# Performance work log

Measured on AMD Instinct MI355X. Metric: run time of the kernel, lower is better.

Reference implementation:

```python
import jax, jax.numpy as jnp
import numpy as np

SEQ, B, D_IN, D_H = 1024, 64, 256, 256


def setup_inputs() -> dict:
    key = jax.random.key(0)
    ks = jax.random.split(key, 9)
    scale = 1.0 / np.sqrt(D_IN + D_H)
    inputs = jax.random.normal(ks[0], (SEQ, B, D_IN), dtype=jnp.float32)
    def lin(k):
        kw, kb = jax.random.split(k)
        W = jax.random.uniform(kw, (D_IN + D_H, D_H), jnp.float32, -scale, scale)
        b = jax.random.uniform(kb, (D_H,), jnp.float32, -scale, scale)
        return W, b
    Wf, bf = lin(ks[1])
    Wi, bi = lin(ks[2])
    Wg, bg = lin(ks[3])
    Wo, bo = lin(ks[4])
    return {"inputs": inputs, "Wf": Wf, "bf": bf, "Wi": Wi, "bi": bi,
            "Wg": Wg, "bg": bg, "Wo": Wo, "bo": bo}


def reference(inputs, Wf, bf, Wi, bi, Wg, bg, Wo, bo):
    B_ = inputs.shape[1]
    hx0 = jnp.zeros((B_, D_H), dtype=inputs.dtype)
    cx0 = jnp.zeros((B_, D_H), dtype=inputs.dtype)

    def step(carry, x):
        hx, cx = carry
        comb = jnp.concatenate([x, hx], axis=1)  # [B, D_IN + D_H]
        f = jax.nn.sigmoid(comb @ Wf + bf)
        i = jax.nn.sigmoid(comb @ Wi + bi)
        g = jnp.tanh(comb @ Wg + bg)
        o = jax.nn.sigmoid(comb @ Wo + bo)
        cx = f * cx + i * g
        hx = o * jnp.tanh(cx)
        return (hx, cx), hx

    (hx, cx), outputs = jax.lax.scan(step, (hx0, cx0), inputs)
    return outputs, hx, cx
```

## Files before the change

kernel.cpp:

```cpp
#include <hip/hip_runtime.h>
#include <hip/hip_bf16.h>


typedef _Float16 f16;
typedef _Float16 f16x4 __attribute__((ext_vector_type(4)));
typedef _Float16 f16x8 __attribute__((ext_vector_type(8)));
typedef float f32x4 __attribute__((ext_vector_type(4)));
typedef int i32x4 __attribute__((ext_vector_type(4)));

#define SEQ 1024
#define BATCH 64
#define DIN 256
#define DH 256
#define NCOL 1024

#define WXP_OFF   0u
#define WHQ_OFF   524288u
#define SCL_OFF   786432u
#define BIAS_OFF  790528u
#define HXS8_OFF  794624u
#define CXS_OFF   811008u
#define XP_OFF    876544u

__device__ __forceinline__ float fast_sigmoid(float x) {
  float e = __expf(-x);
  return __builtin_amdgcn_rcpf(1.0f + e);
}
__device__ __forceinline__ float fast_tanh(float x) {
  x = fminf(fmaxf(x, -15.0f), 15.0f);
  float e = __expf(2.0f * x);
  return (e - 1.0f) * __builtin_amdgcn_rcpf(e + 1.0f);
}
__device__ __forceinline__ void lds_barrier() {
  asm volatile("s_waitcnt lgkmcnt(0)\n\ts_barrier" ::: "memory");
}

__global__ void qlstm_prep(const float* __restrict__ Wf, const float* __restrict__ Wi,
                           const float* __restrict__ Wg, const float* __restrict__ Wo,
                           const float* __restrict__ bf_, const float* __restrict__ bi_,
                           const float* __restrict__ bg_, const float* __restrict__ bo_,
                           f16* __restrict__ Wxp, float* __restrict__ biasp) {
  int tid = blockIdx.x * 256 + threadIdx.x;
  if (tid < 4 * 256 * 256) {
    int g = tid >> 16;
    int rem = tid & 65535;
    int k = rem >> 8, n = rem & 255;
    const float* W = (g == 0) ? Wf : (g == 1) ? Wi : (g == 2) ? Wg : Wo;
    float v = W[k * 256 + n];
    int j = (g << 8) + n;
    Wxp[((size_t)(k >> 3) * 1024 + j) * 8 + (k & 7)] = (f16)v;
  }
  if (tid < 1024) {
    int g = tid >> 8, n = tid & 255;
    const float* bb = (g == 0) ? bf_ : (g == 1) ? bi_ : (g == 2) ? bg_ : bo_;
    biasp[tid] = bb[n];
  }
}

__global__ __launch_bounds__(256) void qlstm_prepq(
    const float* __restrict__ Wf, const float* __restrict__ Wi,
    const float* __restrict__ Wg, const float* __restrict__ Wo,
    char* __restrict__ WhQ, float* __restrict__ scl) {
  int j = blockIdx.x * 256 + threadIdx.x;
  if (j >= 1024) return;
  int g = j >> 8, n = j & 255;
  const float* W = (g == 0) ? Wf : (g == 1) ? Wi : (g == 2) ? Wg : Wo;
  float mx = 0.0f;
  for (int r = 0; r < 256; ++r) mx = fmaxf(mx, fabsf(W[(256 + r) * 256 + n]));
  float s = (mx > 0.0f) ? mx * (1.0f / 127.0f) : 1.0f;
  float inv = 1.0f / s;
  int w = n >> 5, sh = (n >> 4) & 1, c = n & 15, nt = g * 2 + sh;
  size_t tb = ((size_t)(w * 8 + nt) * 4) * 1024;
  for (int kp = 0; kp < 256; ++kp) {
    int r = 32 * (kp >> 5) + ((kp & 31) >> 1) + 16 * (kp & 1);
    float v = W[(256 + r) * 256 + n];
    int q = (int)rintf(v * inv);
    q = q > 127 ? 127 : (q < -127 ? -127 : q);
    int kt = kp >> 6, lane = ((kp >> 4) & 3) * 16 + c, jj = kp & 15;
    WhQ[tb + (size_t)kt * 1024 + lane * 16 + jj] = (char)q;
  }
  scl[j] = s * (1.0f / 127.0f);
}

__global__ __launch_bounds__(256) void qlstm_xproj(
    const float* __restrict__ X, const f16* __restrict__ Wxp,
    const float* __restrict__ biasp, f16* __restrict__ Xp) {
  __shared__ f16 As[128][72];
  __shared__ f16 Bs[8 * 128 * 8];

  int tid = threadIdx.x;
  int tm = blockIdx.x, tn = blockIdx.y;
  int wave = tid >> 6, lane = tid & 63;
  int qm = (wave & 1) * 64, qn = (wave >> 1) * 64;
  int lm = lane & 15, lk = lane >> 4;

  f32x4 acc[4][4];
#pragma unroll
  for (int a = 0; a < 4; ++a)
#pragma unroll
    for (int b = 0; b < 4; ++b) acc[a][b] = (f32x4)0.0f;

  for (int k0 = 0; k0 < 256; k0 += 64) {
    {
      int r = tid >> 1, c0 = (tid & 1) * 32;
      const float4* src = (const float4*)(X + (size_t)(tm * 128 + r) * 256 + k0 + c0);
#pragma unroll
      for (int i = 0; i < 8; ++i) {
        float4 v = src[i];
        f16x4 pk = {(f16)v.x, (f16)v.y, (f16)v.z, (f16)v.w};
        *(f16x4*)&As[r][c0 + i * 4] = pk;
      }
    }
    {
#pragma unroll
      for (int it = 0; it < 4; ++it) {
        int idx = it * 256 + tid;
        int kgi = idx >> 7, n = idx & 127;
        ((uint4*)Bs)[idx] =
            *(const uint4*)(Wxp + (((size_t)(k0 >> 3) + kgi) * 1024 + tn * 128 + n) * 8);
      }
    }
    __syncthreads();
#pragma unroll
    for (int ks = 0; ks < 2; ++ks) {
      f16x8 af[4], bfr[4];
#pragma unroll
      for (int mi = 0; mi < 4; ++mi)
        af[mi] = *(const f16x8*)&As[qm + mi * 16 + lm][ks * 32 + lk * 8];
#pragma unroll
      for (int ni = 0; ni < 4; ++ni)
        bfr[ni] = *(const f16x8*)&Bs[(((ks * 4 + lk) * 128) + qn + ni * 16 + lm) * 8];
#pragma unroll
      for (int mi = 0; mi < 4; ++mi)
#pragma unroll
        for (int ni = 0; ni < 4; ++ni)
          acc[mi][ni] = __builtin_amdgcn_mfma_f32_16x16x32_f16(af[mi], bfr[ni],
                                                               acc[mi][ni], 0, 0, 0);
    }
    __syncthreads();
  }
  int m0 = tm * 128 + qm, j0 = tn * 128 + qn;
#pragma unroll
  for (int mi = 0; mi < 4; ++mi)
#pragma unroll
    for (int ni = 0; ni < 4; ++ni) {
      int j = j0 + ni * 16 + lm;
      float bv = biasp[j];
#pragma unroll
      for (int r = 0; r < 4; ++r) {
        int m = m0 + mi * 16 + lk * 4 + r;
        Xp[(size_t)m * 1024 + j] = (f16)(acc[mi][ni][r] + bv);
      }
    }
}

__device__ __forceinline__ i32x4 MQ(i32x4 a, i32x4 b, i32x4 c) {
  return __builtin_amdgcn_mfma_i32_16x16x64_i8(a, b, c, 0, 0, 0);
}

__global__ __launch_bounds__(512)
__attribute__((amdgpu_waves_per_eu(2, 2))) void qlstm_seq(
    const f16* __restrict__ Xp, const i32x4* __restrict__ WhQ,
    const float* __restrict__ scl,
    float* __restrict__ out, char* __restrict__ hxs8, float* __restrict__ cxs,
    float* __restrict__ hxout, float* __restrict__ cxout, int t0, int t1) {
  __shared__ char hxq[2][256];

  int tid = threadIdx.x;
  int w = tid >> 6, lane = tid & 63, c = lane & 15;
  int b = blockIdx.x;
  int h0 = w * 32 + c, h1 = h0 + 16;

  i32x4 wq[8][4];
  {
    const i32x4* wp = WhQ + (size_t)w * 32 * 64 + lane;
#pragma unroll
    for (int nt = 0; nt < 8; ++nt)
#pragma unroll
      for (int kt = 0; kt < 4; ++kt) wq[nt][kt] = wp[(nt * 4 + kt) * 64];
  }
  float sc[8];
#pragma unroll
  for (int nt = 0; nt < 8; ++nt)
    sc[nt] = scl[(nt >> 1) * 256 + w * 32 + (nt & 1) * 16 + c];

  int par0 = t0 & 1;
  if (tid < 16) {
    uint4 v;
    if (t0 == 0) v = uint4{0u, 0u, 0u, 0u};
    else v = ((const uint4*)(hxs8 + (size_t)b * 256))[tid];
    *(uint4*)(&hxq[par0][tid * 16]) = v;
  }
  float cx0 = 0.0f, cx1 = 0.0f;
  if (t0 != 0) { cx0 = cxs[(size_t)b * 256 + h0]; cx1 = cxs[(size_t)b * 256 + h1]; }

  __syncthreads();

  int koff = (lane >> 4) << 4;
  float hv0 = 0.0f, hv1 = 0.0f;
  for (int t = t0; t < t1; ++t) {
    int par = t & 1, parn = par ^ 1;
    const char* hp = &hxq[par][0];

    const f16* xq = Xp + ((size_t)(t - t0) * BATCH + b) * NCOL;
    f16 xv[8];
#pragma unroll
    for (int nt = 0; nt < 8; ++nt)
      xv[nt] = xq[(nt >> 1) * 256 + w * 32 + (nt & 1) * 16 + c];

    i32x4 acc[8];
#pragma unroll
    for (int nt = 0; nt < 8; ++nt) acc[nt] = i32x4{0, 0, 0, 0};
    i32x4 a0 = *(const i32x4*)(hp + 0 * 64 + koff);
    i32x4 a1 = *(const i32x4*)(hp + 1 * 64 + koff);
#pragma unroll
    for (int nt = 0; nt < 8; ++nt) acc[nt] = MQ(a0, wq[nt][0], acc[nt]);
    a0 = *(const i32x4*)(hp + 2 * 64 + koff);
#pragma unroll
    for (int nt = 0; nt < 8; ++nt) acc[nt] = MQ(a1, wq[nt][1], acc[nt]);
    a1 = *(const i32x4*)(hp + 3 * 64 + koff);
#pragma unroll
    for (int nt = 0; nt < 8; ++nt) acc[nt] = MQ(a0, wq[nt][2], acc[nt]);
#pragma unroll
    for (int nt = 0; nt < 8; ++nt) acc[nt] = MQ(a1, wq[nt][3], acc[nt]);

    float p[8];
#pragma unroll
    for (int nt = 0; nt < 8; ++nt)
      p[nt] = fmaf((float)acc[nt][0], sc[nt], (float)xv[nt]);

    float vf0 = fast_sigmoid(p[0]), vf1 = fast_sigmoid(p[1]);
    float vi0 = fast_sigmoid(p[2]), vi1 = fast_sigmoid(p[3]);
    float vg0 = fast_tanh(p[4]),    vg1 = fast_tanh(p[5]);
    float vo0 = fast_sigmoid(p[6]), vo1 = fast_sigmoid(p[7]);
    cx0 = fmaf(vf0, cx0, vi0 * vg0); hv0 = vo0 * fast_tanh(cx0);
    cx1 = fmaf(vf1, cx1, vi1 * vg1); hv1 = vo1 * fast_tanh(cx1);

    if (lane < 16) {
      float* op = out + ((size_t)t * BATCH + b) * 256;
      op[h0] = hv0; op[h1] = hv1;
    }

    int q0 = (int)rintf(hv0 * 127.0f);
    int q1 = (int)rintf(hv1 * 127.0f);
    unsigned v16 = (unsigned)(q0 & 0xff) | ((unsigned)(q1 & 0xff) << 8);
    unsigned px = (unsigned)__shfl_xor((int)v16, 1, 64);
    unsigned v32 = v16 | (px << 16);
    unsigned py = (unsigned)__shfl_xor((int)v32, 2, 64);
    if (lane < 16 && (lane & 3) == 0)
      *(uint2*)(&hxq[parn][w * 32 + (lane >> 2) * 8]) = uint2{v32, py};

    lds_barrier();
  }

  if (tid < 16)
    ((uint4*)(hxs8 + (size_t)b * 256))[tid] = *(const uint4*)(&hxq[t1 & 1][tid * 16]);
  if (lane < 16) {
    cxs[(size_t)b * 256 + h0] = cx0; cxs[(size_t)b * 256 + h1] = cx1;
    if (t1 == SEQ) {
      hxout[(size_t)b * 256 + h0] = hv0; hxout[(size_t)b * 256 + h1] = hv1;
      cxout[(size_t)b * 256 + h0] = cx0; cxout[(size_t)b * 256 + h1] = cx1;
    }
  }
}

extern "C" void kernel_launch(void* const* d_in, const int* in_sizes, int n_in,
                              void* d_out, int out_size, void* d_ws, size_t ws_size,
                              hipStream_t stream) {
  const float* X  = (const float*)d_in[0];
  const float* Wf = (const float*)d_in[1]; const float* bf_ = (const float*)d_in[2];
  const float* Wi = (const float*)d_in[3]; const float* bi_ = (const float*)d_in[4];
  const float* Wg = (const float*)d_in[5]; const float* bg_ = (const float*)d_in[6];
  const float* Wo = (const float*)d_in[7]; const float* bo_ = (const float*)d_in[8];
  float* out = (float*)d_out;

  char* ws = (char*)d_ws;
  f16*   Wxp   = (f16*)(ws + WXP_OFF);
  char*  WhQ   = (char*)(ws + WHQ_OFF);
  float* scl   = (float*)(ws + SCL_OFF);
  float* biasp = (float*)(ws + BIAS_OFF);
  char*  hxs8  = (char*)(ws + HXS8_OFF);
  float* cxs   = (float*)(ws + CXS_OFF);
  f16*   Xp    = (f16*)(ws + XP_OFF);

  size_t avail = (ws_size > XP_OFF) ? (ws_size - XP_OFF) : 0;
  int Tc = SEQ;
  while (Tc > 2 && (size_t)Tc * BATCH * NCOL * 2 > avail) Tc >>= 1;

  qlstm_prep<<<1024, 256, 0, stream>>>(Wf, Wi, Wg, Wo, bf_, bi_, bg_, bo_,
                                       Wxp, biasp);
  qlstm_prepq<<<4, 256, 0, stream>>>(Wf, Wi, Wg, Wo, WhQ, scl);

  float* hxout = out + (size_t)SEQ * BATCH * DH;
  float* cxout = hxout + BATCH * DH;

  for (int t0 = 0; t0 < SEQ; t0 += Tc) {
    dim3 g1(Tc * BATCH / 128, NCOL / 128);
    qlstm_xproj<<<g1, 256, 0, stream>>>(X + (size_t)t0 * BATCH * DIN, Wxp, biasp, Xp);
    qlstm_seq<<<BATCH, 512, 0, stream>>>(Xp, (const i32x4*)WhQ, scl, out, hxs8, cxs,
                                         hxout, cxout, t0, t0 + Tc);
  }
}
```

Baseline: 1.317 ms.

## Split recurrent LSTM step across 16 waves with gate-interleaved x-projection layout

The sequential kernel now runs 1024 threads (16 waves) per batch row instead of 8 waves, so each wave handles 16 hidden units and issues 16 int8 MFMAs per step instead of 32. The per-step critical path should shrink. The weight-quantization layout is reworked to match, with rows in natural order per gate. The x-projection output is interleaved so the four gate values for each hidden unit sit together and load as a single 8-byte read. The hx int8 store becomes a direct byte write with no shuffles. The cost is more waves taking part in each per-step barrier, and the MFMA work is spread more thinly per wave.

```diff
diff --git a/kernel.cpp b/kernel.cpp
--- a/kernel.cpp
+++ b/kernel.cpp
@@ -33,6 +33,9 @@
 }
 __device__ __forceinline__ void lds_barrier() {
   asm volatile("s_waitcnt lgkmcnt(0)\n\ts_barrier" ::: "memory");
+}
+__device__ __forceinline__ i32x4 MQ(i32x4 a, i32x4 b, i32x4 c) {
+  return __builtin_amdgcn_mfma_i32_16x16x64_i8(a, b, c, 0, 0, 0);
 }
 
 __global__ void qlstm_prep(const float* __restrict__ Wf, const float* __restrict__ Wi,
@@ -69,14 +72,14 @@
   for (int r = 0; r < 256; ++r) mx = fmaxf(mx, fabsf(W[(256 + r) * 256 + n]));
   float s = (mx > 0.0f) ? mx * (1.0f / 127.0f) : 1.0f;
   float inv = 1.0f / s;
-  int w = n >> 5, sh = (n >> 4) & 1, c = n & 15, nt = g * 2 + sh;
-  size_t tb = ((size_t)(w * 8 + nt) * 4) * 1024;
-  for (int kp = 0; kp < 256; ++kp) {
-    int r = 32 * (kp >> 5) + ((kp & 31) >> 1) + 16 * (kp & 1);
+  int w = n >> 4, c = n & 15;
+  size_t tb = (size_t)((w * 4 + g) * 4) * 1024;
+  for (int r = 0; r < 256; ++r) {
     float v = W[(256 + r) * 256 + n];
     int q = (int)rintf(v * inv);
     q = q > 127 ? 127 : (q < -127 ? -127 : q);
-    int kt = kp >> 6, lane = ((kp >> 4) & 3) * 16 + c, jj = kp & 15;
+    int kt = r >> 6, kp = r & 63;
+    int lane = (kp >> 4) * 16 + c, jj = kp & 15;
     WhQ[tb + (size_t)kt * 1024 + lane * 16 + jj] = (char)q;
   }
   scl[j] = s * (1.0f / 127.0f);
@@ -84,7 +87,7 @@
 
 __global__ __launch_bounds__(256) void qlstm_xproj(
     const float* __restrict__ X, const f16* __restrict__ Wxp,
-    const float* __restrict__ biasp, f16* __restrict__ Xp) {
+    const float* __restrict__ biasp, f16* __restrict__ Xp2) {
   __shared__ f16 As[128][72];
   __shared__ f16 Bs[8 * 128 * 8];
 
@@ -145,44 +148,39 @@
 #pragma unroll
     for (int ni = 0; ni < 4; ++ni) {
       int j = j0 + ni * 16 + lm;
+      int gg = j >> 8, hh = j & 255;
       float bv = biasp[j];
 #pragma unroll
       for (int r = 0; r < 4; ++r) {
         int m = m0 + mi * 16 + lk * 4 + r;
-        Xp[(size_t)m * 1024 + j] = (f16)(acc[mi][ni][r] + bv);
+        Xp2[((size_t)m * 256 + hh) * 4 + gg] = (f16)(acc[mi][ni][r] + bv);
       }
     }
 }
 
-__device__ __forceinline__ i32x4 MQ(i32x4 a, i32x4 b, i32x4 c) {
-  return __builtin_amdgcn_mfma_i32_16x16x64_i8(a, b, c, 0, 0, 0);
-}
-
-__global__ __launch_bounds__(512)
-__attribute__((amdgpu_waves_per_eu(2, 2))) void qlstm_seq(
-    const f16* __restrict__ Xp, const i32x4* __restrict__ WhQ,
+__global__ __launch_bounds__(1024, 4) void qlstm_seq(
+    const f16* __restrict__ Xp2, const i32x4* __restrict__ WhQ,
     const float* __restrict__ scl,
     float* __restrict__ out, char* __restrict__ hxs8, float* __restrict__ cxs,
     float* __restrict__ hxout, float* __restrict__ cxout, int t0, int t1) {
   __shared__ char hxq[2][256];
 
   int tid = threadIdx.x;
-  int w = tid >> 6, lane = tid & 63, c = lane & 15;
+  int wv = tid >> 6, lane = tid & 63, c = lane & 15;
   int b = blockIdx.x;
-  int h0 = w * 32 + c, h1 = h0 + 16;
-
-  i32x4 wq[8][4];
+  int h = wv * 16 + c;
+
+  i32x4 wq[4][4];
   {
-    const i32x4* wp = WhQ + (size_t)w * 32 * 64 + lane;
-#pragma unroll
-    for (int nt = 0; nt < 8; ++nt)
-#pragma unroll
-      for (int kt = 0; kt < 4; ++kt) wq[nt][kt] = wp[(nt * 4 + kt) * 64];
-  }
-  float sc[8];
-#pragma unroll
-  for (int nt = 0; nt < 8; ++nt)
-    sc[nt] = scl[(nt >> 1) * 256 + w * 32 + (nt & 1) * 16 + c];
+    const i32x4* wp = WhQ + (size_t)(wv * 16) * 64 + lane;
+#pragma unroll
+    for (int g = 0; g < 4; ++g)
+#pragma unroll
+      for (int kt = 0; kt < 4; ++kt) wq[g][kt] = wp[(g * 4 + kt) * 64];
+  }
+  float sc[4];
+#pragma unroll
+  for (int g = 0; g < 4; ++g) sc[g] = scl[g * 256 + h];
 
   int par0 = t0 & 1;
   if (tid < 16) {
@@ -191,75 +189,59 @@
     else v = ((const uint4*)(hxs8 + (size_t)b * 256))[tid];
     *(uint4*)(&hxq[par0][tid * 16]) = v;
   }
-  float cx0 = 0.0f, cx1 = 0.0f;
-  if (t0 != 0) { cx0 = cxs[(size_t)b * 256 + h0]; cx1 = cxs[(size_t)b * 256 + h1]; }
+  float cx = (t0 != 0) ? cxs[(size_t)b * 256 + h] : 0.0f;
 
   __syncthreads();
 
   int koff = (lane >> 4) << 4;
-  float hv0 = 0.0f, hv1 = 0.0f;
+  float hv = 0.0f;
   for (int t = t0; t < t1; ++t) {
     int par = t & 1, parn = par ^ 1;
     const char* hp = &hxq[par][0];
 
-    const f16* xq = Xp + ((size_t)(t - t0) * BATCH + b) * NCOL;
-    f16 xv[8];
-#pragma unroll
-    for (int nt = 0; nt < 8; ++nt)
-      xv[nt] = xq[(nt >> 1) * 256 + w * 32 + (nt & 1) * 16 + c];
-
-    i32x4 acc[8];
-#pragma unroll
-    for (int nt = 0; nt < 8; ++nt) acc[nt] = i32x4{0, 0, 0, 0};
-    i32x4 a0 = *(const i32x4*)(hp + 0 * 64 + koff);
-    i32x4 a1 = *(const i32x4*)(hp + 1 * 64 + koff);
-#pragma unroll
-    for (int nt = 0; nt < 8; ++nt) acc[nt] = MQ(a0, wq[nt][0], acc[nt]);
-    a0 = *(const i32x4*)(hp + 2 * 64 + koff);
-#pragma unroll
-    for (int nt = 0; nt < 8; ++nt) acc[nt] = MQ(a1, wq[nt][1], acc[nt]);
-    a1 = *(const i32x4*)(hp + 3 * 64 + koff);
-#pragma unroll
-    for (int nt = 0; nt < 8; ++nt) acc[nt] = MQ(a0, wq[nt][2], acc[nt]);
-#pragma unroll
-    for (int nt = 0; nt < 8; ++nt) acc[nt] = MQ(a1, wq[nt][3], acc[nt]);
-
-    float p[8];
-#pragma unroll
-    for (int nt = 0; nt < 8; ++nt)
-      p[nt] = fmaf((float)acc[nt][0], sc[nt], (float)xv[nt]);
-
-    float vf0 = fast_sigmoid(p[0]), vf1 = fast_sigmoid(p[1]);
-    float vi0 = fast_sigmoid(p[2]), vi1 = fast_sigmoid(p[3]);
-    float vg0 = fast_tanh(p[4]),    vg1 = fast_tanh(p[5]);
-    float vo0 = fast_sigmoid(p[6]), vo1 = fast_sigmoid(p[7]);
-    cx0 = fmaf(vf0, cx0, vi0 * vg0); hv0 = vo0 * fast_tanh(cx0);
-    cx1 = fmaf(vf1, cx1, vi1 * vg1); hv1 = vo1 * fast_tanh(cx1);
+    uint2 xr = *(const uint2*)(Xp2 + (((size_t)(t - t0) * BATCH + b) * 256 + h) * 4);
+
+    i32x4 acc0{}, acc1{}, acc2{}, acc3{};
+    i32x4 a0 = *(const i32x4*)(hp + koff);
+    i32x4 a1 = *(const i32x4*)(hp + 64 + koff);
+    acc0 = MQ(a0, wq[0][0], acc0); acc1 = MQ(a0, wq[1][0], acc1);
+    acc2 = MQ(a0, wq[2][0], acc2); acc3 = MQ(a0, wq[3][0], acc3);
+    a0 = *(const i32x4*)(hp + 128 + koff);
+    acc0 = MQ(a1, wq[0][1], acc0); acc1 = MQ(a1, wq[1][1], acc1);
+    acc2 = MQ(a1, wq[2][1], acc2); acc3 = MQ(a1, wq[3][1], acc3);
+    a1 = *(const i32x4*)(hp + 192 + koff);
+    acc0 = MQ(a0, wq[0][2], acc0); acc1 = MQ(a0, wq[1][2], acc1);
+    acc2 = MQ(a0, wq[2][2], acc2); acc3 = MQ(a0, wq[3][2], acc3);
+    acc0 = MQ(a1, wq[0][3], acc0); acc1 = MQ(a1, wq[1][3], acc1);
+    acc2 = MQ(a1, wq[2][3], acc2); acc3 = MQ(a1, wq[3][3], acc3);
+
+    f16x4 xh = __builtin_bit_cast(f16x4, xr);
+    float p0 = fmaf((float)acc0[0], sc[0], (float)xh[0]);
+    float p1 = fmaf((float)acc1[0], sc[1], (float)xh[1]);
+    float p2 = fmaf((float)acc2[0], sc[2], (float)xh[2]);
+    float p3 = fmaf((float)acc3[0], sc[3], (float)xh[3]);
+
+    float vf = fast_sigmoid(p0);
+    float vi = fast_sigmoid(p1);
+    float vg = fast_tanh(p2);
+    float vo = fast_sigmoid(p3);
+    cx = fmaf(vf, cx, vi * vg);
+    hv = vo * fast_tanh(cx);
 
     if (lane < 16) {
-      float* op = out + ((size_t)t * BATCH + b) * 256;
-      op[h0] = hv0; op[h1] = hv1;
-    }
-
-    int q0 = (int)rintf(hv0 * 127.0f);
-    int q1 = (int)rintf(hv1 * 127.0f);
-    unsigned v16 = (unsigned)(q0 & 0xff) | ((unsigned)(q1 & 0xff) << 8);
-    unsigned px = (unsigned)__shfl_xor((int)v16, 1, 64);
-    unsigned v32 = v16 | (px << 16);
-    unsigned py = (unsigned)__shfl_xor((int)v32, 2, 64);
-    if (lane < 16 && (lane & 3) == 0)
-      *(uint2*)(&hxq[parn][w * 32 + (lane >> 2) * 8]) = uint2{v32, py};
-
+      out[((size_t)t * BATCH + b) * 256 + h] = hv;
+      hxq[parn][h] = (char)(int)rintf(hv * 127.0f);
+    }
     lds_barrier();
   }
 
   if (tid < 16)
     ((uint4*)(hxs8 + (size_t)b * 256))[tid] = *(const uint4*)(&hxq[t1 & 1][tid * 16]);
   if (lane < 16) {
-    cxs[(size_t)b * 256 + h0] = cx0; cxs[(size_t)b * 256 + h1] = cx1;
+    cxs[(size_t)b * 256 + h] = cx;
     if (t1 == SEQ) {
-      hxout[(size_t)b * 256 + h0] = hv0; hxout[(size_t)b * 256 + h1] = hv1;
-      cxout[(size_t)b * 256 + h0] = cx0; cxout[(size_t)b * 256 + h1] = cx1;
+      hxout[(size_t)b * 256 + h] = hv;
+      cxout[(size_t)b * 256 + h] = cx;
     }
   }
 }
@@ -281,7 +263,7 @@
   float* biasp = (float*)(ws + BIAS_OFF);
   char*  hxs8  = (char*)(ws + HXS8_OFF);
   float* cxs   = (float*)(ws + CXS_OFF);
-  f16*   Xp    = (f16*)(ws + XP_OFF);
+  f16*   Xp2   = (f16*)(ws + XP_OFF);
 
   size_t avail = (ws_size > XP_OFF) ? (ws_size - XP_OFF) : 0;
   int Tc = SEQ;
@@ -296,8 +278,8 @@
 
   for (int t0 = 0; t0 < SEQ; t0 += Tc) {
     dim3 g1(Tc * BATCH / 128, NCOL / 128);
-    qlstm_xproj<<<g1, 256, 0, stream>>>(X + (size_t)t0 * BATCH * DIN, Wxp, biasp, Xp);
-    qlstm_seq<<<BATCH, 512, 0, stream>>>(Xp, (const i32x4*)WhQ, scl, out, hxs8, cxs,
-                                         hxout, cxout, t0, t0 + Tc);
-  }
-}
+    qlstm_xproj<<<g1, 256, 0, stream>>>(X + (size_t)t0 * BATCH * DIN, Wxp, biasp, Xp2);
+    qlstm_seq<<<BATCH, 1024, 0, stream>>>(Xp2, (const i32x4*)WhQ, scl, out, hxs8, cxs,
+                                          hxout, cxout, t0, t0 + Tc);
+  }
+}
```

After: 1.319 ms. About the same (+0.2%).
